# Kernel optimization log

Measured on AMD Instinct MI355X. Metric: run time of the kernel, lower is better.

Reference implementation:

```python
import jax, jax.numpy as jnp
import numpy as np

B, C, H, W = 4, 512, 64, 64
CH = C // 2  # 256


def setup_inputs() -> dict:
    key = jax.random.key(0)
    ks = jax.random.split(key, 10)
    s = 0.02  # keep logits in sane range for softmax
    return {
        "Fc": jax.random.normal(ks[0], (B, C, H, W), jnp.float32),
        "Fs": jax.random.normal(ks[1], (B, C, H, W), jnp.float32),
        "f_w": jax.random.normal(ks[2], (CH, C), jnp.float32) * s,
        "f_b": jax.random.normal(ks[3], (CH,), jnp.float32) * s,
        "g_w": jax.random.normal(ks[4], (CH, C), jnp.float32) * s,
        "g_b": jax.random.normal(ks[5], (CH,), jnp.float32) * s,
        "h_w": jax.random.normal(ks[6], (C, C), jnp.float32) * s,
        "h_b": jax.random.normal(ks[7], (C,), jnp.float32) * s,
        "out_w": jax.random.normal(ks[8], (C, C), jnp.float32) * s,
        "out_b": jax.random.normal(ks[9], (C,), jnp.float32) * s,
    }


def _conv1x1(x, w, b):
    # x: [B,C,H,W], w: [O,C], b: [O] -> [B,O,H,W]
    return jnp.einsum('oc,bchw->bohw', w, x) + b[None, :, None, None]


def reference(Fc, Fs, f_w, f_b, g_w, g_b, h_w, h_b, out_w, out_b):
    b, c, h, w = Fc.shape
    hw = h * w
    Ff = _conv1x1(Fc, f_w, f_b).reshape(b, -1, hw)   # [B, C/2, HW]
    Fg = _conv1x1(Fs, g_w, g_b).reshape(b, -1, hw)   # [B, C/2, HW]
    Fh = _conv1x1(Fs, h_w, h_b).reshape(b, -1, hw)   # [B, C,   HW]
    d_k = Ff.shape[1]  # channels//2, matches torch d_k after permute
    # Attention[b,i,j] over style positions j
    logits = jnp.einsum('bci,bcj->bij', Ff, Fg) / jnp.sqrt(jnp.float32(d_k))
    attn = jax.nn.softmax(logits, axis=-1)           # [B, HW, HW]
    # Out[b,c,i] = sum_j Fh[b,c,j] * attn[b,i,j]
    out = jnp.einsum('bcj,bij->bci', Fh, attn).reshape(b, c, h, w)
    return _conv1x1(out, out_w, out_b) + Fc
```

## Files before the change

### kernel.cpp

```cpp
#include <hip/hip_runtime.h>
#include <hip/hip_bf16.h>

#define HW    4096
#define CDIM  512
#define CHALF 256
#define NB    4
#define FLASH_LDS 99328
#define MERGE_LDS 66048

using bf16 = __hip_bfloat16;
typedef __attribute__((ext_vector_type(8))) short short8;
typedef __attribute__((ext_vector_type(4))) float float4v;

typedef __attribute__((address_space(1))) void gvoid_t;
typedef __attribute__((address_space(3))) void svoid_t;
#define GLD16(gp, lp) \
    __builtin_amdgcn_global_load_lds((gvoid_t*)(gp), (svoid_t*)(lp), 16, 0, 0)
#define MFMA(a, b, c) __builtin_amdgcn_mfma_f32_16x16x32_bf16(a, b, c, 0, 0, 0)

static __device__ __forceinline__ short8 ld_short8(const bf16* p) {
    return *reinterpret_cast<const short8*>(p);
}
static __device__ __forceinline__ float b2f(short s) {
    unsigned u = ((unsigned)(unsigned short)s) << 16;
    return __builtin_bit_cast(float, u);
}
static __device__ __forceinline__ short f2bs(float f) {
    bf16 h = __float2bfloat16(f);
    return __builtin_bit_cast(short, h);
}

__global__ void transpose_cast(const float* __restrict__ Fc,
                               const float* __restrict__ Fs,
                               bf16* __restrict__ FcT, bf16* __restrict__ FsT) {
    __shared__ float tile[32][33];
    int p0 = blockIdx.x * 32, c0 = blockIdx.y * 32;
    int z = blockIdx.z;
    int b = z & 3, which = z >> 2;
    const float* src = (which ? Fs : Fc) + (size_t)b * CDIM * HW;
    bf16* dst = (which ? FsT : FcT) + (size_t)b * HW * CDIM;
    int tx = threadIdx.x, ty = threadIdx.y;
    for (int i = 0; i < 4; i++)
        tile[ty + 8 * i][tx] = src[(size_t)(c0 + ty + 8 * i) * HW + p0 + tx];
    __syncthreads();
    for (int i = 0; i < 4; i++)
        dst[(size_t)(p0 + ty + 8 * i) * CDIM + c0 + tx] =
            __float2bfloat16(tile[tx][ty + 8 * i]);
}

__global__ void cast4(const float* __restrict__ fw, const float* __restrict__ gw,
                      const float* __restrict__ hw, const float* __restrict__ ow,
                      bf16* __restrict__ dst) {
    int i = blockIdx.x * 256 + threadIdx.x;
    float v;
    if (i < 131072)       v = fw[i] * 0.0625f;
    else if (i < 262144)  v = gw[i - 131072];
    else if (i < 524288)  v = hw[i - 262144];
    else                  v = ow[i - 524288];
    dst[i] = __float2bfloat16(v);
}

__launch_bounds__(256, 2)
__global__ void gemm_fg(const bf16* __restrict__ A1, const bf16* __restrict__ A2,
                        size_t sA,
                        const bf16* __restrict__ W1, const bf16* __restrict__ W2,
                        const float* __restrict__ b1, const float* __restrict__ b2,
                        float bs1, float bs2,
                        bf16* __restrict__ D1, bf16* __restrict__ D2, size_t sD,
                        int zhalf, int N, int K) {
    __shared__ bf16 Asf[2][8192];
    __shared__ bf16 Bsf[2][8192];
    int lid = blockIdx.x;
    int xcd = lid & 7, idx = lid >> 3;
    int bx = idx & 1;
    int yzg = xcd * 32 + (idx >> 1);
    int z = yzg >> 5;
    int by = yzg & 31;
    const bf16 *A, *W; const float* bias; float bsc; bf16* D;
    if (z < zhalf) { A = A1 + sA * z;           W = W1; bias = b1; bsc = bs1; D = D1 + sD * z; }
    else           { A = A2 + sA * (z - zhalf); W = W2; bias = b2; bsc = bs2; D = D2 + sD * (z - zhalf); }
    int m0 = by * 128, n0 = bx * 128;
    int t = threadIdx.x;
    int w = t >> 6, lane = t & 63;
    int wm = w >> 1, wn = w & 1;
    int l15 = lane & 15, quad = lane >> 4;
    int lr = lane >> 3, lc = (lane & 7) ^ lr;
    int nk = K >> 6;
    float4v acc[4][4] = {};

    for (int q = 0; q < 4; q++) {
        int rb = w * 32 + q * 8;
        GLD16(A + (size_t)(m0 + rb + lr) * K + lc * 8, &Asf[0][rb * 64]);
        GLD16(W + (size_t)(n0 + rb + lr) * K + lc * 8, &Bsf[0][rb * 64]);
    }
    for (int i = 0; i < nk; i++) {
        __syncthreads();
        if (i + 1 < nk) {
            int k0 = (i + 1) << 6, nb = (i + 1) & 1;
            for (int q = 0; q < 4; q++) {
                int rb = w * 32 + q * 8;
                GLD16(A + (size_t)(m0 + rb + lr) * K + k0 + lc * 8, &Asf[nb][rb * 64]);
                GLD16(W + (size_t)(n0 + rb + lr) * K + k0 + lc * 8, &Bsf[nb][rb * 64]);
            }
        }
        int cb = i & 1;
        for (int h = 0; h < 2; h++) {
            int p = (h * 4 + quad) ^ (l15 & 7);
            short8 af[4], bfr[4];
            for (int sm = 0; sm < 4; sm++)
                af[sm] = *(const short8*)&Asf[cb][(wm * 64 + sm * 16 + l15) * 64 + p * 8];
            for (int sn = 0; sn < 4; sn++)
                bfr[sn] = *(const short8*)&Bsf[cb][(wn * 64 + sn * 16 + l15) * 64 + p * 8];
            for (int sm = 0; sm < 4; sm++)
                for (int sn = 0; sn < 4; sn++)
                    acc[sm][sn] = MFMA(af[sm], bfr[sn], acc[sm][sn]);
        }
    }
    for (int sm = 0; sm < 4; sm++)
        for (int sn = 0; sn < 4; sn++) {
            int n = n0 + wn * 64 + sn * 16 + l15;
            for (int r = 0; r < 4; r++) {
                int m = m0 + wm * 64 + sm * 16 + quad * 4 + r;
                D[(size_t)m * N + n] = __float2bfloat16(acc[sm][sn][r] + bias[n] * bsc);
            }
        }
}

__launch_bounds__(256, 2)
__global__ void gemm_bw(const bf16* __restrict__ Aw,
                        const bf16* __restrict__ Bact, size_t sB,
                        const float* __restrict__ bias,
                        bf16* __restrict__ Dp, size_t sD,
                        int N, int K) {
    __shared__ bf16 Asf[2][8192];
    __shared__ bf16 Bsf[2][8192];
    int lid = blockIdx.x;
    int xcd = lid & 7, idx = lid >> 3;
    int my = idx & 3;
    int nzg = xcd * 16 + (idx >> 2);
    int z = nzg >> 5;
    int nx = nzg & 31;
    const bf16* A = Aw;
    const bf16* Bm = Bact + sB * z;
    int m0 = my * 128, n0 = nx * 128;
    int t = threadIdx.x;
    int w = t >> 6, lane = t & 63;
    int wm = w >> 1, wn = w & 1;
    int l15 = lane & 15, quad = lane >> 4;
    int lr = lane >> 3, lc = (lane & 7) ^ lr;
    int nk = K >> 6;
    float4v acc[4][4] = {};

    for (int q = 0; q < 4; q++) {
        int rb = w * 32 + q * 8;
        GLD16(A + (size_t)(m0 + rb + lr) * K + lc * 8, &Asf[0][rb * 64]);
        GLD16(Bm + (size_t)(n0 + rb + lr) * K + lc * 8, &Bsf[0][rb * 64]);
    }
    for (int i = 0; i < nk; i++) {
        __syncthreads();
        if (i + 1 < nk) {
            int k0 = (i + 1) << 6, nb = (i + 1) & 1;
            for (int q = 0; q < 4; q++) {
                int rb = w * 32 + q * 8;
                GLD16(A + (size_t)(m0 + rb + lr) * K + k0 + lc * 8, &Asf[nb][rb * 64]);
                GLD16(Bm + (size_t)(n0 + rb + lr) * K + k0 + lc * 8, &Bsf[nb][rb * 64]);
            }
        }
        int cb = i & 1;
        for (int h = 0; h < 2; h++) {
            int p = (h * 4 + quad) ^ (l15 & 7);
            short8 af[4], bfr[4];
            for (int sm = 0; sm < 4; sm++)
                af[sm] = *(const short8*)&Asf[cb][(wm * 64 + sm * 16 + l15) * 64 + p * 8];
            for (int sn = 0; sn < 4; sn++)
                bfr[sn] = *(const short8*)&Bsf[cb][(wn * 64 + sn * 16 + l15) * 64 + p * 8];
            for (int sm = 0; sm < 4; sm++)
                for (int sn = 0; sn < 4; sn++)
                    acc[sm][sn] = MFMA(af[sm], bfr[sn], acc[sm][sn]);
        }
    }
    for (int sm = 0; sm < 4; sm++)
        for (int sn = 0; sn < 4; sn++) {
            int n = n0 + wn * 64 + sn * 16 + l15;
            for (int r = 0; r < 4; r++) {
                int m = m0 + wm * 64 + sm * 16 + quad * 4 + r;
                Dp[sD * z + (size_t)m * N + n] =
                    __float2bfloat16(acc[sm][sn][r] + bias[m]);
            }
        }
}

__launch_bounds__(512, 1)
__global__ void flash_attn(const bf16* __restrict__ Q_, const bf16* __restrict__ Kt_,
                           const bf16* __restrict__ V_,
                           bf16* __restrict__ O0_, bf16* __restrict__ O1_,
                           float* __restrict__ L0_, float* __restrict__ L1_) {
    extern __shared__ char smem[];
    bf16* Ksf = (bf16*)smem;
    short* Ps = (short*)(smem + 65536);
    float* lpart = (float*)(smem + 98304);

    int lid = blockIdx.x;
    int stream = lid & 7;
    int b = stream & 3, jh = stream >> 2;
    int i0 = (lid >> 3) * 128;
    const bf16* Kt = Kt_ + (size_t)b * HW * CHALF;
    const bf16* V  = V_ + (size_t)b * CDIM * HW;
    bf16* Out   = (jh ? O1_ : O0_) + ((size_t)b * HW + i0) * CDIM;
    float* Lout = (jh ? L1_ : L0_) + (size_t)b * HW + i0;

    int t = threadIdx.x;
    int w = t >> 6, lane = t & 63;
    int l15 = lane & 15, quad = lane >> 4;
    int rm   = (w & 3) * 32;
    int cnw  = (w >> 2) * 32;
    int chb  = (w >> 2) * 4;
    int c0w  = w * 64;
    int jbeg = jh * (HW / 2), jend = jbeg + HW / 2;

    short8 qf0[8], qf1[8];
    {
        const bf16* qp = Q_ + ((size_t)b * HW + i0 + rm + l15) * CHALF + quad * 8;
        #pragma unroll
        for (int k8 = 0; k8 < 8; k8++) {
            qf0[k8] = ld_short8(qp + k8 * 32);
            qf1[k8] = ld_short8(qp + 16 * CHALF + k8 * 32);
        }
    }
    int r0 = lane >> 5, cc = lane & 31;

    for (int i = 0; i < 4; i++) {
        int rp = i * 8 + w;
        int r = 2 * rp + r0;
        int c = cc ^ (r & 7);
        GLD16(Kt + (size_t)(jbeg + r) * CHALF + c * 8, &Ksf[rp * 512]);
    }
    float l_lane[2][4] = {};
    float4v oacc[8][4] = {};
    asm volatile("s_waitcnt vmcnt(0)" ::: "memory");
    __builtin_amdgcn_s_barrier();

    const bf16* vp = V + (size_t)(c0w + l15) * HW + quad * 8;
    short8 va[4];

    auto qksm = [&](int kb) {
        const bf16* Kb = Ksf + kb * 16384;
        short* Pb = Ps + kb * 8192;
        float4v s00 = {}, s01 = {}, s10 = {}, s11 = {};
        __builtin_amdgcn_s_setprio(1);
        #pragma unroll
        for (int k8 = 0; k8 < 8; k8++) {
            int pq = ((k8 * 4 + quad) ^ (l15 & 7)) * 8;
            short8 k0 = *(const short8*)&Kb[(cnw + l15) * 256 + pq];
            short8 k1 = *(const short8*)&Kb[(cnw + 16 + l15) * 256 + pq];
            s00 = MFMA(qf0[k8], k0, s00);
            s01 = MFMA(qf0[k8], k1, s01);
            s10 = MFMA(qf1[k8], k0, s10);
            s11 = MFMA(qf1[k8], k1, s11);
        }
        __builtin_amdgcn_s_setprio(0);
        #pragma unroll
        for (int r = 0; r < 4; r++) {
            int rl0 = rm + quad * 4 + r, rl1 = rl0 + 16;
            int cw = chb + (l15 >> 3);
            float p00 = __expf(s00[r]);
            float p01 = __expf(s01[r]);
            float p10 = __expf(s10[r]);
            float p11 = __expf(s11[r]);
            l_lane[0][r] += p00 + p01;
            l_lane[1][r] += p10 + p11;
            Pb[rl0 * 64 + ((cw + rl0) & 7) * 8 + (l15 & 7)]     = f2bs(p00);
            Pb[rl0 * 64 + ((cw + 2 + rl0) & 7) * 8 + (l15 & 7)] = f2bs(p01);
            Pb[rl1 * 64 + ((cw + rl1) & 7) * 8 + (l15 & 7)]     = f2bs(p10);
            Pb[rl1 * 64 + ((cw + 2 + rl1) & 7) * 8 + (l15 & 7)] = f2bs(p11);
        }
    };
    auto pvhalf = [&](int pb, int coff, const short8* vv) {
        __builtin_amdgcn_s_setprio(1);
        #pragma unroll
        for (int sm = 0; sm < 8; sm++) {
            int rl = sm * 16 + l15;
            short8 pf = *(const short8*)&Ps[pb * 8192 + rl * 64 +
                                            ((coff + quad + rl) & 7) * 8];
            #pragma unroll
            for (int sn = 0; sn < 4; sn++)
                oacc[sm][sn] = MFMA(pf, vv[sn], oacc[sm][sn]);
        }
        __builtin_amdgcn_s_setprio(0);
    };

    for (int i = 0; i < 4; i++) {
        int rp = i * 8 + w;
        int r = 2 * rp + r0;
        int c = cc ^ (r & 7);
        GLD16(Kt + (size_t)(jbeg + 64 + r) * CHALF + c * 8,
              &Ksf[16384 + rp * 512]);
    }
    #pragma unroll
    for (int sn = 0; sn < 4; sn++)
        va[sn] = ld_short8(vp + jbeg + (size_t)(sn * 16) * HW);
    qksm(0);
    asm volatile("s_waitcnt lgkmcnt(0)" ::: "memory");
    asm volatile("s_waitcnt vmcnt(4)" ::: "memory");
    __builtin_amdgcn_s_barrier();

    for (int it = 1; it < 32; it++) {
        int j0 = jbeg + it * 64, jp = j0 - 64;
        int pb = (it - 1) & 1, kb = it & 1;
        short8 vb[4];
        #pragma unroll
        for (int sn = 0; sn < 4; sn++)
            vb[sn] = ld_short8(vp + jp + 32 + (size_t)(sn * 16) * HW);
        if (it < 31) {
            for (int i = 0; i < 4; i++) {
                int rp = i * 8 + w;
                int r = 2 * rp + r0;
                int c = cc ^ (r & 7);
                GLD16(Kt + (size_t)(j0 + 64 + r) * CHALF + c * 8,
                      &Ksf[(kb ^ 1) * 16384 + rp * 512]);
            }
        }
        pvhalf(pb, 0, va);
        __builtin_amdgcn_sched_barrier(0);
        #pragma unroll
        for (int sn = 0; sn < 4; sn++)
            va[sn] = ld_short8(vp + j0 + (size_t)(sn * 16) * HW);
        pvhalf(pb, 4, vb);
        qksm(kb);
        asm volatile("s_waitcnt lgkmcnt(0)" ::: "memory");
        asm volatile("s_waitcnt vmcnt(4)" ::: "memory");
        __builtin_amdgcn_s_barrier();
    }

    {
        short8 vb[4];
        int jp = jend - 64;
        #pragma unroll
        for (int sn = 0; sn < 4; sn++)
            vb[sn] = ld_short8(vp + jp + 32 + (size_t)(sn * 16) * HW);
        pvhalf(1, 0, va);
        pvhalf(1, 4, vb);
    }

    #pragma unroll
    for (int ms = 0; ms < 2; ms++)
        for (int r = 0; r < 4; r++) {
            float red = l_lane[ms][r];
            red += __shfl_xor(red, 1);
            red += __shfl_xor(red, 2);
            red += __shfl_xor(red, 4);
            red += __shfl_xor(red, 8);
            if (l15 == 0)
                lpart[(w >> 2) * 128 + rm + ms * 16 + quad * 4 + r] = red;
        }
    __syncthreads();
    if ((w >> 2) == 0 && l15 == 0)
        for (int ms = 0; ms < 2; ms++)
            for (int r = 0; r < 4; r++) {
                int rl = rm + ms * 16 + quad * 4 + r;
                Lout[rl] = lpart[rl] + lpart[128 + rl];
            }
    for (int sm = 0; sm < 8; sm++)
        for (int r = 0; r < 4; r++) {
            int rl = sm * 16 + quad * 4 + r;
            float li = 1.0f / (lpart[rl] + lpart[128 + rl]);
            for (int sn = 0; sn < 4; sn++)
                Out[(size_t)rl * CDIM + c0w + sn * 16 + l15] =
                    __float2bfloat16(oacc[sm][sn][r] * li);
        }
}

__launch_bounds__(256, 1)
__global__ void merge_out(const bf16* __restrict__ Op0, const bf16* __restrict__ Op1,
                          const float* __restrict__ L0, const float* __restrict__ L1,
                          const bf16* __restrict__ ow, const float* __restrict__ out_b,
                          const float* __restrict__ Fc, float* __restrict__ out) {
    extern __shared__ char smem[];
    short* Os = (short*)smem;
    float* lw = (float*)(smem + 65536);

    int rt = blockIdx.x;
    int b = rt >> 6;
    int i0 = (rt & 63) * 64;
    size_t obase = ((size_t)b * HW + i0) * CDIM;
    int t = threadIdx.x;

    if (t < 64) {
        float l0 = L0[(size_t)b * HW + i0 + t];
        float l1 = L1[(size_t)b * HW + i0 + t];
        float inv = 1.f / (l0 + l1);
        lw[t * 2] = l0 * inv;
        lw[t * 2 + 1] = l1 * inv;
    }
    __syncthreads();

    for (int q = 0; q < 16; q++) {
        int idx = q * 256 + t;
        int row = idx >> 6, cc = idx & 63;
        short8 a = ld_short8(Op0 + obase + (size_t)row * CDIM + cc * 8);
        short8 c = ld_short8(Op1 + obase + (size_t)row * CDIM + cc * 8);
        float w0 = lw[row * 2], w1 = lw[row * 2 + 1];
        short8 o;
        #pragma unroll
        for (int j = 0; j < 8; j++)
            o[j] = f2bs(w0 * b2f(a[j]) + w1 * b2f(c[j]));
        *(short8*)&Os[row * 512 + (cc ^ (row & 7)) * 8] = o;
    }
    __syncthreads();

    int w = t >> 6, lane = t & 63;
    int l15 = lane & 15, quad = lane >> 4;
    int m0 = w * 128;
    float4v acc[8][4] = {};
    for (int k8 = 0; k8 < 16; k8++) {
        short8 bfr[4];
        #pragma unroll
        for (int n16 = 0; n16 < 4; n16++)
            bfr[n16] = *(const short8*)&Os[(n16 * 16 + l15) * 512 +
                (((k8 * 4 + quad) ^ (l15 & 7))) * 8];
        short8 af[8];
        #pragma unroll
        for (int m16 = 0; m16 < 8; m16++)
            af[m16] = ld_short8(ow + (size_t)(m0 + m16 * 16 + l15) * CDIM +
                                k8 * 32 + quad * 8);
        #pragma unroll
        for (int m16 = 0; m16 < 8; m16++)
            for (int n16 = 0; n16 < 4; n16++)
                acc[m16][n16] = MFMA(af[m16], bfr[n16], acc[m16][n16]);
    }

    const float* fcb = Fc + (size_t)b * CDIM * HW;
    float* outb = out + (size_t)b * CDIM * HW;
    for (int m16 = 0; m16 < 8; m16++)
        for (int r = 0; r < 4; r++) {
            int co = m0 + m16 * 16 + quad * 4 + r;
            float bb = out_b[co];
            for (int n16 = 0; n16 < 4; n16++) {
                int i = i0 + n16 * 16 + l15;
                outb[(size_t)co * HW + i] =
                    acc[m16][n16][r] + bb + fcb[(size_t)co * HW + i];
            }
        }
}

extern "C" void kernel_launch(void* const* d_in, const int* in_sizes, int n_in,
                              void* d_out, int out_size, void* d_ws, size_t ws_size,
                              hipStream_t stream) {
    const float* Fc   = (const float*)d_in[0];
    const float* Fs   = (const float*)d_in[1];
    const float* f_w  = (const float*)d_in[2];
    const float* f_b  = (const float*)d_in[3];
    const float* g_w  = (const float*)d_in[4];
    const float* g_b  = (const float*)d_in[5];
    const float* h_w  = (const float*)d_in[6];
    const float* h_b  = (const float*)d_in[7];
    const float* out_w = (const float*)d_in[8];
    const float* out_b = (const float*)d_in[9];
    float* out = (float*)d_out;

    bf16* FcT = (bf16*)d_ws;
    bf16* FsT = FcT + (size_t)NB * HW * CDIM;
    bf16* FfT = FsT + (size_t)NB * HW * CDIM;
    bf16* FgT = FfT + (size_t)NB * HW * CHALF;
    bf16* Fh  = FgT + (size_t)NB * HW * CHALF;
    bf16* fw  = Fh  + (size_t)NB * CDIM * HW;
    bf16* gw  = fw + (size_t)CHALF * CDIM;
    bf16* hw  = gw + (size_t)CHALF * CDIM;
    bf16* ow  = hw + (size_t)CDIM * CDIM;
    float* L0 = (float*)(ow + (size_t)CDIM * CDIM);
    float* L1 = L0 + (size_t)NB * HW;
    bf16* Op0 = FcT;
    bf16* Op1 = FsT;

    hipFuncSetAttribute((const void*)flash_attn,
                        hipFuncAttributeMaxDynamicSharedMemorySize, FLASH_LDS);
    hipFuncSetAttribute((const void*)merge_out,
                        hipFuncAttributeMaxDynamicSharedMemorySize, MERGE_LDS);

    transpose_cast<<<dim3(HW / 32, CDIM / 32, NB * 2), dim3(32, 8), 0, stream>>>(
        Fc, Fs, FcT, FsT);
    cast4<<<dim3(786432 / 256), 256, 0, stream>>>(f_w, g_w, h_w, out_w, fw);

    gemm_fg<<<dim3(512), 256, 0, stream>>>(
        FcT, FsT, (size_t)HW * CDIM, fw, gw, f_b, g_b, 0.0625f, 1.0f,
        FfT, FgT, (size_t)HW * CHALF, NB, CHALF, CDIM);
    gemm_bw<<<dim3(512), 256, 0, stream>>>(
        hw, FsT, (size_t)HW * CDIM, h_b, Fh, (size_t)CDIM * HW, HW, CDIM);
    flash_attn<<<dim3(256), 512, FLASH_LDS, stream>>>(
        FfT, FgT, Fh, Op0, Op1, L0, L1);
    merge_out<<<dim3(256), 256, MERGE_LDS, stream>>>(
        Op0, Op1, L0, L1, ow, out_b, Fc, out);
}
```

Before: 370.9 us.

## Merge projection GEMMs into one launch and halve merge_out row tile

The two projection GEMM kernels (Ff/Fg and Fh) are folded into a single 1024-block launch that picks its role from the block index. This removes one launch and lets both GEMMs share the machine at the same time instead of running back to back. merge_out now handles 32 rows per block instead of 64, with half the LDS, a 2-block occupancy bound and twice as many blocks, to improve occupancy. The trade-off is that each merge block reloads the full out_w weight for less work, so weight traffic doubles.

```diff
diff --git a/kernel.cpp b/kernel.cpp
--- a/kernel.cpp
+++ b/kernel.cpp
@@ -6,7 +6,7 @@
 #define CHALF 256
 #define NB    4
 #define FLASH_LDS 99328
-#define MERGE_LDS 66048
+#define MERGE_LDS 33024
 
 using bf16 = __hip_bfloat16;
 typedef __attribute__((ext_vector_type(8))) short short8;
@@ -61,25 +61,45 @@
 }
 
 __launch_bounds__(256, 2)
-__global__ void gemm_fg(const bf16* __restrict__ A1, const bf16* __restrict__ A2,
-                        size_t sA,
-                        const bf16* __restrict__ W1, const bf16* __restrict__ W2,
-                        const float* __restrict__ b1, const float* __restrict__ b2,
-                        float bs1, float bs2,
-                        bf16* __restrict__ D1, bf16* __restrict__ D2, size_t sD,
-                        int zhalf, int N, int K) {
+__global__ void gemm_all(const bf16* __restrict__ FcT, const bf16* __restrict__ FsT,
+                         const bf16* __restrict__ fw, const bf16* __restrict__ gw,
+                         const bf16* __restrict__ hww,
+                         const float* __restrict__ f_b, const float* __restrict__ g_b,
+                         const float* __restrict__ h_b,
+                         bf16* __restrict__ FfT, bf16* __restrict__ FgT,
+                         bf16* __restrict__ Fh) {
     __shared__ bf16 Asf[2][8192];
     __shared__ bf16 Bsf[2][8192];
+    const int K = CDIM;
     int lid = blockIdx.x;
-    int xcd = lid & 7, idx = lid >> 3;
-    int bx = idx & 1;
-    int yzg = xcd * 32 + (idx >> 1);
-    int z = yzg >> 5;
-    int by = yzg & 31;
-    const bf16 *A, *W; const float* bias; float bsc; bf16* D;
-    if (z < zhalf) { A = A1 + sA * z;           W = W1; bias = b1; bsc = bs1; D = D1 + sD * z; }
-    else           { A = A2 + sA * (z - zhalf); W = W2; bias = b2; bsc = bs2; D = D2 + sD * (z - zhalf); }
-    int m0 = by * 128, n0 = bx * 128;
+    int xcd = lid & 7;
+    int rest = lid >> 3;
+    int which = rest & 1;
+    int idx = rest >> 1;
+
+    const bf16 *Arow, *Brow;
+    const float* bias; float bsc; bf16* D; int N; int m0, n0; int bias_on_m;
+    if (which == 0) {
+        int bx = idx & 1;
+        int yzg = xcd * 32 + (idx >> 1);
+        int z = yzg >> 5;
+        int by = yzg & 31;
+        size_t sA = (size_t)HW * CDIM, sD = (size_t)HW * CHALF;
+        if (z < NB) { Arow = FcT + sA * z;        Brow = fw; bias = f_b; bsc = 0.0625f; D = FfT + sD * z; }
+        else        { Arow = FsT + sA * (z - NB); Brow = gw; bias = g_b; bsc = 1.0f;    D = FgT + sD * (z - NB); }
+        m0 = by * 128; n0 = bx * 128; N = CHALF; bias_on_m = 0;
+    } else {
+        int my = idx & 3;
+        int nzg = xcd * 16 + (idx >> 2);
+        int z = nzg >> 5;
+        int nx = nzg & 31;
+        Arow = hww;
+        Brow = FsT + (size_t)HW * CDIM * z;
+        bias = h_b; bsc = 1.0f;
+        D = Fh + (size_t)CDIM * HW * z;
+        m0 = my * 128; n0 = nx * 128; N = HW; bias_on_m = 1;
+    }
+
     int t = threadIdx.x;
     int w = t >> 6, lane = t & 63;
     int wm = w >> 1, wn = w & 1;
@@ -90,8 +110,8 @@
 
     for (int q = 0; q < 4; q++) {
         int rb = w * 32 + q * 8;
-        GLD16(A + (size_t)(m0 + rb + lr) * K + lc * 8, &Asf[0][rb * 64]);
-        GLD16(W + (size_t)(n0 + rb + lr) * K + lc * 8, &Bsf[0][rb * 64]);
+        GLD16(Arow + (size_t)(m0 + rb + lr) * K + lc * 8, &Asf[0][rb * 64]);
+        GLD16(Brow + (size_t)(n0 + rb + lr) * K + lc * 8, &Bsf[0][rb * 64]);
     }
     for (int i = 0; i < nk; i++) {
         __syncthreads();
@@ -99,8 +119,8 @@
             int k0 = (i + 1) << 6, nb = (i + 1) & 1;
             for (int q = 0; q < 4; q++) {
                 int rb = w * 32 + q * 8;
-                GLD16(A + (size_t)(m0 + rb + lr) * K + k0 + lc * 8, &Asf[nb][rb * 64]);
-                GLD16(W + (size_t)(n0 + rb + lr) * K + k0 + lc * 8, &Bsf[nb][rb * 64]);
+                GLD16(Arow + (size_t)(m0 + rb + lr) * K + k0 + lc * 8, &Asf[nb][rb * 64]);
+                GLD16(Brow + (size_t)(n0 + rb + lr) * K + k0 + lc * 8, &Bsf[nb][rb * 64]);
             }
         }
         int cb = i & 1;
@@ -121,71 +141,8 @@
             int n = n0 + wn * 64 + sn * 16 + l15;
             for (int r = 0; r < 4; r++) {
                 int m = m0 + wm * 64 + sm * 16 + quad * 4 + r;
-                D[(size_t)m * N + n] = __float2bfloat16(acc[sm][sn][r] + bias[n] * bsc);
-            }
-        }
-}
-
-__launch_bounds__(256, 2)
-__global__ void gemm_bw(const bf16* __restrict__ Aw,
-                        const bf16* __restrict__ Bact, size_t sB,
-                        const float* __restrict__ bias,
-                        bf16* __restrict__ Dp, size_t sD,
-                        int N, int K) {
-    __shared__ bf16 Asf[2][8192];
-    __shared__ bf16 Bsf[2][8192];
-    int lid = blockIdx.x;
-    int xcd = lid & 7, idx = lid >> 3;
-    int my = idx & 3;
-    int nzg = xcd * 16 + (idx >> 2);
-    int z = nzg >> 5;
-    int nx = nzg & 31;
-    const bf16* A = Aw;
-    const bf16* Bm = Bact + sB * z;
-    int m0 = my * 128, n0 = nx * 128;
-    int t = threadIdx.x;
-    int w = t >> 6, lane = t & 63;
-    int wm = w >> 1, wn = w & 1;
-    int l15 = lane & 15, quad = lane >> 4;
-    int lr = lane >> 3, lc = (lane & 7) ^ lr;
-    int nk = K >> 6;
-    float4v acc[4][4] = {};
-
-    for (int q = 0; q < 4; q++) {
-        int rb = w * 32 + q * 8;
-        GLD16(A + (size_t)(m0 + rb + lr) * K + lc * 8, &Asf[0][rb * 64]);
-        GLD16(Bm + (size_t)(n0 + rb + lr) * K + lc * 8, &Bsf[0][rb * 64]);
-    }
-    for (int i = 0; i < nk; i++) {
-        __syncthreads();
-        if (i + 1 < nk) {
-            int k0 = (i + 1) << 6, nb = (i + 1) & 1;
-            for (int q = 0; q < 4; q++) {
-                int rb = w * 32 + q * 8;
-                GLD16(A + (size_t)(m0 + rb + lr) * K + k0 + lc * 8, &Asf[nb][rb * 64]);
-                GLD16(Bm + (size_t)(n0 + rb + lr) * K + k0 + lc * 8, &Bsf[nb][rb * 64]);
-            }
-        }
-        int cb = i & 1;
-        for (int h = 0; h < 2; h++) {
-            int p = (h * 4 + quad) ^ (l15 & 7);
-            short8 af[4], bfr[4];
-            for (int sm = 0; sm < 4; sm++)
-                af[sm] = *(const short8*)&Asf[cb][(wm * 64 + sm * 16 + l15) * 64 + p * 8];
-            for (int sn = 0; sn < 4; sn++)
-                bfr[sn] = *(const short8*)&Bsf[cb][(wn * 64 + sn * 16 + l15) * 64 + p * 8];
-            for (int sm = 0; sm < 4; sm++)
-                for (int sn = 0; sn < 4; sn++)
-                    acc[sm][sn] = MFMA(af[sm], bfr[sn], acc[sm][sn]);
-        }
-    }
-    for (int sm = 0; sm < 4; sm++)
-        for (int sn = 0; sn < 4; sn++) {
-            int n = n0 + wn * 64 + sn * 16 + l15;
-            for (int r = 0; r < 4; r++) {
-                int m = m0 + wm * 64 + sm * 16 + quad * 4 + r;
-                Dp[sD * z + (size_t)m * N + n] =
-                    __float2bfloat16(acc[sm][sn][r] + bias[m]);
+                float bb = bias_on_m ? bias[m] : bias[n] * bsc;
+                D[(size_t)m * N + n] = __float2bfloat16(acc[sm][sn][r] + bb);
             }
         }
 }
@@ -370,22 +327,22 @@
         }
 }
 
-__launch_bounds__(256, 1)
+__launch_bounds__(256, 2)
 __global__ void merge_out(const bf16* __restrict__ Op0, const bf16* __restrict__ Op1,
                           const float* __restrict__ L0, const float* __restrict__ L1,
                           const bf16* __restrict__ ow, const float* __restrict__ out_b,
                           const float* __restrict__ Fc, float* __restrict__ out) {
     extern __shared__ char smem[];
     short* Os = (short*)smem;
-    float* lw = (float*)(smem + 65536);
+    float* lw = (float*)(smem + 32768);
 
     int rt = blockIdx.x;
-    int b = rt >> 6;
-    int i0 = (rt & 63) * 64;
+    int b = rt >> 7;
+    int i0 = (rt & 127) * 32;
     size_t obase = ((size_t)b * HW + i0) * CDIM;
     int t = threadIdx.x;
 
-    if (t < 64) {
+    if (t < 32) {
         float l0 = L0[(size_t)b * HW + i0 + t];
         float l1 = L1[(size_t)b * HW + i0 + t];
         float inv = 1.f / (l0 + l1);
@@ -394,7 +351,7 @@
     }
     __syncthreads();
 
-    for (int q = 0; q < 16; q++) {
+    for (int q = 0; q < 8; q++) {
         int idx = q * 256 + t;
         int row = idx >> 6, cc = idx & 63;
         short8 a = ld_short8(Op0 + obase + (size_t)row * CDIM + cc * 8);
@@ -411,11 +368,11 @@
     int w = t >> 6, lane = t & 63;
     int l15 = lane & 15, quad = lane >> 4;
     int m0 = w * 128;
-    float4v acc[8][4] = {};
+    float4v acc[8][2] = {};
     for (int k8 = 0; k8 < 16; k8++) {
-        short8 bfr[4];
-        #pragma unroll
-        for (int n16 = 0; n16 < 4; n16++)
+        short8 bfr[2];
+        #pragma unroll
+        for (int n16 = 0; n16 < 2; n16++)
             bfr[n16] = *(const short8*)&Os[(n16 * 16 + l15) * 512 +
                 (((k8 * 4 + quad) ^ (l15 & 7))) * 8];
         short8 af[8];
@@ -425,7 +382,7 @@
                                 k8 * 32 + quad * 8);
         #pragma unroll
         for (int m16 = 0; m16 < 8; m16++)
-            for (int n16 = 0; n16 < 4; n16++)
+            for (int n16 = 0; n16 < 2; n16++)
                 acc[m16][n16] = MFMA(af[m16], bfr[n16], acc[m16][n16]);
     }
 
@@ -435,7 +392,7 @@
         for (int r = 0; r < 4; r++) {
             int co = m0 + m16 * 16 + quad * 4 + r;
             float bb = out_b[co];
-            for (int n16 = 0; n16 < 4; n16++) {
+            for (int n16 = 0; n16 < 2; n16++) {
                 int i = i0 + n16 * 16 + l15;
                 outb[(size_t)co * HW + i] =
                     acc[m16][n16][r] + bb + fcb[(size_t)co * HW + i];
@@ -481,13 +438,10 @@
         Fc, Fs, FcT, FsT);
     cast4<<<dim3(786432 / 256), 256, 0, stream>>>(f_w, g_w, h_w, out_w, fw);
 
-    gemm_fg<<<dim3(512), 256, 0, stream>>>(
-        FcT, FsT, (size_t)HW * CDIM, fw, gw, f_b, g_b, 0.0625f, 1.0f,
-        FfT, FgT, (size_t)HW * CHALF, NB, CHALF, CDIM);
-    gemm_bw<<<dim3(512), 256, 0, stream>>>(
-        hw, FsT, (size_t)HW * CDIM, h_b, Fh, (size_t)CDIM * HW, HW, CDIM);
+    gemm_all<<<dim3(1024), 256, 0, stream>>>(
+        FcT, FsT, fw, gw, hw, f_b, g_b, h_b, FfT, FgT, Fh);
     flash_attn<<<dim3(256), 512, FLASH_LDS, stream>>>(
         FfT, FgT, Fh, Op0, Op1, L0, L1);
-    merge_out<<<dim3(256), 256, MERGE_LDS, stream>>>(
+    merge_out<<<dim3(512), 256, MERGE_LDS, stream>>>(
         Op0, Op1, L0, L1, ow, out_b, Fc, out);
 }
```

Result: slower. 391.0 us (+5.4%).
